# Optimization experiments

Hardware: AMD Instinct MI355X
Metric: run time of the kernel (lower is better)

The kernel has to match this reference:

```python
import jax, jax.numpy as jnp
import numpy as np

B, H, W, C = 8, 128, 128, 192
NH, WS, SHIFT = 6, 8, 4
N = WS * WS          # tokens per window = 64
NWIN = (H // WS) * (W // WS)  # 256 windows per image
SCALE = (C // NH) ** -0.5
EPS = 1e-5

# ---- relative position index (static, numpy) ----
_c = np.stack(np.meshgrid(np.arange(WS), np.arange(WS), indexing='ij')).reshape(2, -1)
_r = (_c[:, :, None] - _c[:, None, :]).transpose(1, 2, 0).astype(np.int64)
_r[..., 0] += WS - 1
_r[..., 1] += WS - 1
_r[..., 0] *= 2 * WS - 1
REL_IDX = jnp.asarray(_r.sum(-1))  # (N, N) in [0, (2*WS-1)**2)

# ---- shifted-window attention mask (static, numpy) ----
_img = np.zeros((H, W))
_cnt = 0
for hs in (slice(0, -WS), slice(-WS, -SHIFT), slice(-SHIFT, None)):
    for ws_ in (slice(0, -WS), slice(-WS, -SHIFT), slice(-SHIFT, None)):
        _img[hs, ws_] = _cnt
        _cnt += 1
_img = _img.reshape(H // WS, WS, W // WS, WS).transpose(0, 2, 1, 3).reshape(-1, N)
_m = _img[:, None, :] - _img[:, :, None]
ATTN_MASK = jnp.asarray(np.where(_m != 0, -100.0, 0.0).astype(np.float32))  # (NWIN, N, N)


def layer_norm(x, w, b):
    mu = x.mean(-1, keepdims=True)
    var = ((x - mu) ** 2).mean(-1, keepdims=True)  # biased variance
    return (x - mu) / jnp.sqrt(var + EPS) * w + b


def window_partition(x):
    # (B, H, W, C) -> (B*NWIN, N, C)
    x = x.reshape(B, H // WS, WS, W // WS, WS, C)
    return x.transpose(0, 1, 3, 2, 4, 5).reshape(B * NWIN, N, C)


def window_reverse(w_):
    # (B*NWIN, N, C) -> (B, H, W, C)
    x = w_.reshape(B, H // WS, W // WS, WS, WS, C)
    return x.transpose(0, 1, 3, 2, 4, 5).reshape(B, H, W, C)


def setup_inputs() -> dict:
    key = jax.random.key(0)
    ks = jax.random.split(key, 6)
    return {
        'x': jax.random.normal(ks[0], (B, H * W, C), jnp.float32),
        'ln1_w': jnp.ones((C,), jnp.float32),
        'ln1_b': jnp.zeros((C,), jnp.float32),
        'qkv_w': jax.random.normal(ks[1], (C, 3 * C), jnp.float32) * 0.02,
        'qkv_b': jnp.zeros((3 * C,), jnp.float32),
        'rpb_table': jax.random.normal(ks[2], ((2 * WS - 1) ** 2, NH), jnp.float32) * 0.02,
        'proj_w': jax.random.normal(ks[3], (C, C), jnp.float32) * 0.02,
        'proj_b': jnp.zeros((C,), jnp.float32),
        'ln2_w': jnp.ones((C,), jnp.float32),
        'ln2_b': jnp.zeros((C,), jnp.float32),
        'fc1_w': jax.random.normal(ks[4], (C, 4 * C), jnp.float32) * 0.02,
        'fc1_b': jnp.zeros((4 * C,), jnp.float32),
        'fc2_w': jax.random.normal(ks[5], (4 * C, C), jnp.float32) * 0.02,
        'fc2_b': jnp.zeros((C,), jnp.float32),
    }


def reference(x, ln1_w, ln1_b, qkv_w, qkv_b, rpb_table, proj_w, proj_b,
              ln2_w, ln2_b, fc1_w, fc1_b, fc2_w, fc2_b):
    shortcut = x
    h = layer_norm(x, ln1_w, ln1_b).reshape(B, H, W, C)
    # cyclic shift
    h = jnp.roll(h, shift=(-SHIFT, -SHIFT), axis=(1, 2))
    xw = window_partition(h)  # (B*NWIN, N, C)

    qkv = (xw @ qkv_w + qkv_b).reshape(B * NWIN, N, 3, NH, C // NH)
    q, k, v = [qkv[:, :, i].transpose(0, 2, 1, 3) for i in range(3)]  # (Bn, NH, N, hd)
    attn = jnp.einsum('bhqd,bhkd->bhqk', q * SCALE, k)  # (Bn, NH, N, N)

    rel_bias = rpb_table[REL_IDX].transpose(2, 0, 1)  # (NH, N, N)
    attn = attn + rel_bias[None]
    # shift mask: broadcast per window
    attn = attn.reshape(B, NWIN, NH, N, N) + ATTN_MASK[None, :, None]
    attn = jax.nn.softmax(attn.reshape(B * NWIN, NH, N, N), axis=-1)

    out = jnp.einsum('bhqk,bhkd->bhqd', attn, v)
    out = out.transpose(0, 2, 1, 3).reshape(B * NWIN, N, C)
    out = out @ proj_w + proj_b

    h = window_reverse(out)
    h = jnp.roll(h, shift=(SHIFT, SHIFT), axis=(1, 2)).reshape(B, H * W, C)
    x = shortcut + h

    # MLP
    m = layer_norm(x, ln2_w, ln2_b)
    m = jax.nn.gelu(m @ fc1_w + fc1_b, approximate=False) @ fc2_w + fc2_b
    return x + m
```

## Files before the change

kernel.cpp:

```cpp
#include <hip/hip_runtime.h>
#include <math.h>

typedef _Float16 f16;
typedef _Float16 f16x8 __attribute__((ext_vector_type(8)));
typedef float f32x4 __attribute__((ext_vector_type(4)));

namespace {
constexpr int Hh = 128, Ww = 128, Cc = 192;
constexpr int NHh = 6;
constexpr int Nn = 64, HDd = 32;
constexpr int SH = 4;
constexpr int Mrows = 131072;
constexpr int NWINtot = 2048;
constexpr float LNEPS = 1e-5f;
constexpr float QSCALE = 0.17677669529663687f;
}

__device__ __forceinline__ void ldsload16(const void* g, void* l) {
  __builtin_amdgcn_global_load_lds(
      (const __attribute__((address_space(1))) void*)g,
      (__attribute__((address_space(3))) void*)l, 16, 0, 0);
}

__device__ __forceinline__ int win_row_to_src(int m) {
  int tok = m & 63;
  int wi  = m >> 6;
  int ww = wi & 15, wh = (wi >> 4) & 15, b = wi >> 8;
  int r = (wh << 3) + (tok >> 3);
  int c = (ww << 3) + (tok & 7);
  int ro = (r + SH) & (Hh - 1);
  int co = (c + SH) & (Ww - 1);
  return (b << 14) + (ro << 7) + co;
}

template <int GATHER>
__global__ __launch_bounds__(256) void ln_prep_kernel(
    const float* __restrict__ X, const float* __restrict__ lnw,
    const float* __restrict__ lnb, f16* __restrict__ outh, int m0) {
  __shared__ float xr[16][192];
  __shared__ float smu[16], srs[16];
  __shared__ int src[16];
  const int t = threadIdx.x;
  const int r0 = blockIdx.x * 16;
  if (t < 16) {
    int m = m0 + r0 + t;
    src[t] = GATHER ? win_row_to_src(m) : m;
  }
  __syncthreads();
#pragma unroll
  for (int it = 0; it < 3; ++it) {
    int f = t + it * 256;
    int row = f / 48, c4 = f - row * 48;
    float4 v = *(const float4*)&X[(size_t)src[row] * 192 + c4 * 4];
    *(float4*)&xr[row][c4 * 4] = v;
  }
  __syncthreads();
  {
    const int lane = t & 63, w = t >> 6;
    const int g = lane >> 4, li = lane & 15;
    const int row = w * 4 + g;
    float s = 0.f, s2 = 0.f;
#pragma unroll
    for (int j = 0; j < 12; ++j) {
      float v = xr[row][li + j * 16];
      s += v; s2 += v * v;
    }
#pragma unroll
    for (int off = 1; off < 16; off <<= 1) {
      s += __shfl_xor(s, off);
      s2 += __shfl_xor(s2, off);
    }
    if (li == 0) {
      float m = s * (1.f / 192.f);
      smu[row] = m;
      srs[row] = rsqrtf(s2 * (1.f / 192.f) - m * m + LNEPS);
    }
  }
  __syncthreads();
#pragma unroll
  for (int it = 0; it < 2; ++it) {
    int c = t + it * 256;
    if (c < 384) {
      int e0 = c * 8;
      int row = e0 / 192, col = e0 - row * 192;
      float mu_ = smu[row], rs_ = srs[row];
      f16x8 o;
#pragma unroll
      for (int j = 0; j < 8; ++j) {
        float v = (xr[row][col + j] - mu_) * rs_ * lnw[col + j] + lnb[col + j];
        o[j] = (f16)v;
      }
      *(f16x8*)&outh[(size_t)(m0 + r0) * 192 + e0] = o;
    }
  }
}

__global__ __launch_bounds__(256) void rpb_expand_kernel(
    const float* __restrict__ rpb, float* __restrict__ biasF2) {
  int t = blockIdx.x * 256 + threadIdx.x;
  if (t >= NHh * 4 * 4 * 64 * 4) return;
  int r = t & 3, lane = (t >> 2) & 63, jt = (t >> 8) & 3, it = (t >> 10) & 3, h = t >> 12;
  int row = it * 16 + (lane >> 4) * 4 + r;
  int col = jt * 16 + (lane & 15);
  int dh = (row >> 3) - (col >> 3) + 7;
  int dw = (row & 7) - (col & 7) + 7;
  biasF2[t] = rpb[(dh * 15 + dw) * NHh + h];
}

__global__ __launch_bounds__(256) void wconv_frag(
    const float* __restrict__ W, f16* __restrict__ Wf, int K, int N) {
  int tid = blockIdx.x * 256 + threadIdx.x;
  if (tid >= K * N) return;
  int e = tid & 7, lane = (tid >> 3) & 63, f = tid >> 9;
  int NKT = K >> 5;
  int kt = f % NKT, nt = f / NKT;
  int k = kt * 32 + ((lane >> 4) << 3) + e;
  int n = nt * 16 + (lane & 15);
  Wf[tid] = (f16)W[(size_t)k * N + n];
}

template <int KDIM, int NDIM, int EMODE>
__global__ __launch_bounds__(512, 2) void gemm_mfma16(
    const f16* __restrict__ Abase, const f16* __restrict__ Bf,
    const float* __restrict__ bias, const float* __restrict__ resid,
    void* __restrict__ outp, int m0a, int m0e, int nbx) {
  constexpr int NCH = KDIM / 192;
  constexpr int NKT = KDIM / 32;
  __shared__ __align__(16) char lds[48 * 1024];

  const int tid = threadIdx.x;
  const int lane = tid & 63;
  const int wid = tid >> 6;
  const int wr = wid & 1, wc = wid >> 1;
  const int l15 = lane & 15, g2 = lane >> 4;

  int b = blockIdx.x;
  const int nb = gridDim.x;
  if ((nb & 7) == 0) b = (b & 7) * (nb >> 3) + (b >> 3);
  const int bx = b % nbx;
  const int by = b / nbx;
  const int bn = bx * 192;
  const int bm = by * 128;
  const int nt0 = bx * 12 + wc * 3;

  const int srow = tid >> 2;
  const int kq = tid & 3;
  const int sg = srow >> 4;
  const int slot = srow & 15;
  const f16* arow = Abase + (size_t)(m0a + bm + srow) * KDIM;

  f32x4 acc[4][3];
#pragma unroll
  for (int i = 0; i < 4; ++i)
#pragma unroll
    for (int j = 0; j < 3; ++j) acc[i][j] = (f32x4){0.f, 0.f, 0.f, 0.f};

  for (int c = 0; c < NCH; ++c) {
    if (c) __syncthreads();
#pragma unroll
    for (int u = 0; u < 6; ++u) {
      int ch = kq + u * 4;
      f16x8 v = *(const f16x8*)&arow[c * 192 + ch * 8];
      int ks = ch >> 2, h = ch & 3;
      *(f16x8*)(lds + (ks * 8 + sg) * 1024 + (slot + h * 16) * 16) = v;
    }
    __syncthreads();

#pragma unroll
    for (int ks = 0; ks < 6; ++ks) {
      f16x8 bf[3];
#pragma unroll
      for (int ni = 0; ni < 3; ++ni)
        bf[ni] = *(const f16x8*)&Bf[
            (((size_t)(nt0 + ni) * NKT + (c * 6 + ks)) << 9) + (lane << 3)];
#pragma unroll
      for (int mi = 0; mi < 4; ++mi) {
        f16x8 ah = *(const f16x8*)(lds + (ks * 8 + wr * 4 + mi) * 1024 + lane * 16);
#pragma unroll
        for (int ni = 0; ni < 3; ++ni)
          acc[mi][ni] = __builtin_amdgcn_mfma_f32_16x16x32_f16(ah, bf[ni], acc[mi][ni], 0, 0, 0);
      }
    }
  }

#pragma unroll
  for (int mi = 0; mi < 4; ++mi) {
#pragma unroll
    for (int ni = 0; ni < 3; ++ni) {
      int col = bn + wc * 48 + ni * 16 + l15;
      float bcol = bias[col];
#pragma unroll
      for (int r = 0; r < 4; ++r) {
        int ml = bm + wr * 64 + mi * 16 + g2 * 4 + r;
        float v = acc[mi][ni][r] + bcol;
        if (EMODE == 0) {
          ((f16*)outp)[(size_t)ml * NDIM + col] = (f16)v;
        } else {
          int dst = win_row_to_src(m0e + ml);
          ((float*)outp)[(size_t)dst * NDIM + col] = v + resid[(size_t)dst * NDIM + col];
        }
      }
    }
  }
}

__global__ __launch_bounds__(256, 2) void mlp_fused(
    const f16* __restrict__ oh, const f16* __restrict__ W1f,
    const f16* __restrict__ W2f, const float* __restrict__ b1,
    const float* __restrict__ b2, float* __restrict__ out) {
  __shared__ __align__(16) char ldsA[24 * 1024];
  __shared__ __align__(16) char ldsH[24 * 1024];

  const int tid = threadIdx.x;
  const int lane = tid & 63;
  const int wc = tid >> 6;
  const int l15 = lane & 15, g2 = lane >> 4;
  const int bm = blockIdx.x * 64;

  {
    const f16* src = oh + (size_t)(bm + wc * 16 + l15) * 192 + g2 * 8;
#pragma unroll
    for (int ks = 0; ks < 6; ++ks)
      ldsload16(src + ks * 32, &ldsA[(ks * 4 + wc) * 1024]);
  }

  f32x4 acc2[4][3];
#pragma unroll
  for (int i = 0; i < 4; ++i)
#pragma unroll
    for (int j = 0; j < 3; ++j) acc2[i][j] = (f32x4){0.f, 0.f, 0.f, 0.f};

  __syncthreads();

  for (int hc = 0; hc < 4; ++hc) {
    f32x4 acc1[4][3];
#pragma unroll
    for (int i = 0; i < 4; ++i)
#pragma unroll
      for (int j = 0; j < 3; ++j) acc1[i][j] = (f32x4){0.f, 0.f, 0.f, 0.f};
#pragma unroll
    for (int ks = 0; ks < 6; ++ks) {
      f16x8 bf[3];
#pragma unroll
      for (int ni = 0; ni < 3; ++ni)
        bf[ni] = *(const f16x8*)&W1f[
            (((size_t)(hc * 12 + wc * 3 + ni) * 6 + ks) << 9) + (lane << 3)];
#pragma unroll
      for (int mi = 0; mi < 4; ++mi) {
        f16x8 ah = *(const f16x8*)(ldsA + (ks * 4 + mi) * 1024 + lane * 16);
#pragma unroll
        for (int ni = 0; ni < 3; ++ni)
          acc1[mi][ni] = __builtin_amdgcn_mfma_f32_16x16x32_f16(ah, bf[ni], acc1[mi][ni], 0, 0, 0);
      }
    }
#pragma unroll
    for (int mi = 0; mi < 4; ++mi)
#pragma unroll
      for (int ni = 0; ni < 3; ++ni) {
        float bcol = b1[hc * 192 + wc * 48 + ni * 16 + l15];
#pragma unroll
        for (int r = 0; r < 4; ++r) {
          float v = acc1[mi][ni][r] + bcol;
          float u = v * (1.f + 0.044715f * v * v);
          float ex = __expf(-1.5957691216f * u);
          v = v * __builtin_amdgcn_rcpf(1.f + ex);
          int row = mi * 16 + g2 * 4 + r;
          int col = wc * 48 + ni * 16 + l15;
          *(f16*)(ldsH + ((col >> 5) * 4 + mi) * 1024 +
                  ((row & 15) + ((col >> 3) & 3) * 16) * 16 + (col & 7) * 2) = (f16)v;
        }
      }
    __syncthreads();

#pragma unroll
    for (int ks = 0; ks < 6; ++ks) {
      f16x8 bf[3];
#pragma unroll
      for (int ni = 0; ni < 3; ++ni)
        bf[ni] = *(const f16x8*)&W2f[
            (((size_t)(wc * 3 + ni) * 24 + hc * 6 + ks) << 9) + (lane << 3)];
#pragma unroll
      for (int mi = 0; mi < 4; ++mi) {
        f16x8 ah = *(const f16x8*)(ldsH + (ks * 4 + mi) * 1024 + lane * 16);
#pragma unroll
        for (int ni = 0; ni < 3; ++ni)
          acc2[mi][ni] = __builtin_amdgcn_mfma_f32_16x16x32_f16(ah, bf[ni], acc2[mi][ni], 0, 0, 0);
      }
    }
    __syncthreads();
  }

#pragma unroll
  for (int mi = 0; mi < 4; ++mi)
#pragma unroll
    for (int ni = 0; ni < 3; ++ni) {
      int col = wc * 48 + ni * 16 + l15;
      float bcol = b2[col];
#pragma unroll
      for (int r = 0; r < 4; ++r) {
        int ml = bm + mi * 16 + g2 * 4 + r;
        out[(size_t)ml * 192 + col] = acc2[mi][ni][r] + bcol + out[(size_t)ml * 192 + col];
      }
    }
}

__global__ __launch_bounds__(384) void attn_mfma(
    const f16* __restrict__ qkv, const float* __restrict__ biasF2,
    f16* __restrict__ out, int w0) {
  __shared__ f16 Vt[192 * 64];
  __shared__ f16 Pb[NHh][64 * 64];
  const int t = threadIdx.x;
  const int h = t >> 6;
  const int lane = t & 63;
  const int g = lane >> 4, l15 = lane & 15;
  const int wl = blockIdx.x;
  const f16* base = qkv + (size_t)wl * 64 * 576;

  {
    const f16* vr = base + (size_t)lane * 576 + 384 + h * 32;
    f16x8 vv[4];
#pragma unroll
    for (int u = 0; u < 4; ++u) vv[u] = *(const f16x8*)&vr[u * 8];
    const int c = lane >> 3, e7 = lane & 7;
#pragma unroll
    for (int u = 0; u < 4; ++u)
#pragma unroll
      for (int e = 0; e < 8; ++e) {
        int d = h * 32 + u * 8 + e;
        Vt[d * 64 + ((c ^ e) << 3) + e7] = vv[u][e];
      }
  }

  f16x8 qf[4], kf[4];
#pragma unroll
  for (int it = 0; it < 4; ++it)
    qf[it] = *(const f16x8*)&base[(size_t)(it * 16 + l15) * 576 + h * 32 + g * 8];
#pragma unroll
  for (int jt = 0; jt < 4; ++jt)
    kf[jt] = *(const f16x8*)&base[(size_t)(jt * 16 + l15) * 576 + 192 + h * 32 + g * 8];

  f32x4 S[4][4];
#pragma unroll
  for (int it = 0; it < 4; ++it)
#pragma unroll
    for (int jt = 0; jt < 4; ++jt) S[it][jt] = (f32x4){0.f, 0.f, 0.f, 0.f};
#pragma unroll
  for (int it = 0; it < 4; ++it)
#pragma unroll
    for (int jt = 0; jt < 4; ++jt)
      S[it][jt] = __builtin_amdgcn_mfma_f32_16x16x32_f16(qf[it], kf[jt], S[it][jt], 0, 0, 0);

  const int wi = (w0 + wl) & 255;
  const int wh = wi >> 4, wwc = wi & 15;
  int regj[4];
#pragma unroll
  for (int jt = 0; jt < 4; ++jt) {
    int col = jt * 16 + l15;
    int rj = wh * 8 + (col >> 3), cj = wwc * 8 + (col & 7);
    regj[jt] = (rj < 120 ? 0 : rj < 124 ? 1 : 2) * 3 + (cj < 120 ? 0 : cj < 124 ? 1 : 2);
  }
#pragma unroll
  for (int it = 0; it < 4; ++it) {
    int regi[4];
#pragma unroll
    for (int r = 0; r < 4; ++r) {
      int row = it * 16 + g * 4 + r;
      int ri = wh * 8 + (row >> 3), ci = wwc * 8 + (row & 7);
      regi[r] = (ri < 120 ? 0 : ri < 124 ? 1 : 2) * 3 + (ci < 120 ? 0 : ci < 124 ? 1 : 2);
    }
#pragma unroll
    for (int jt = 0; jt < 4; ++jt) {
      f32x4 bb = *(const f32x4*)&biasF2[(((h * 4 + it) * 4 + jt) * 64 + lane) * 4];
#pragma unroll
      for (int r = 0; r < 4; ++r) {
        float v = S[it][jt][r] * QSCALE + bb[r];
        if (regi[r] != regj[jt]) v -= 100.f;
        S[it][jt][r] = v;
      }
    }
  }

#pragma unroll
  for (int it = 0; it < 4; ++it) {
#pragma unroll
    for (int r = 0; r < 4; ++r) {
      float m = fmaxf(fmaxf(S[it][0][r], S[it][1][r]), fmaxf(S[it][2][r], S[it][3][r]));
#pragma unroll
      for (int off = 1; off < 16; off <<= 1) m = fmaxf(m, __shfl_xor(m, off));
#pragma unroll
      for (int jt = 0; jt < 4; ++jt) S[it][jt][r] = __expf(S[it][jt][r] - m);
    }
  }

  f16* pb = &Pb[h][0];
#pragma unroll
  for (int it = 0; it < 4; ++it)
#pragma unroll
    for (int jt = 0; jt < 4; ++jt)
#pragma unroll
      for (int r = 0; r < 4; ++r) {
        int row = it * 16 + g * 4 + r;
        int cs = (jt * 2 + (l15 >> 3)) ^ (row & 7);
        pb[row * 64 + cs * 8 + (l15 & 7)] = (f16)S[it][jt][r];
      }

  f32x4 O[4][2], Ssum[4];
#pragma unroll
  for (int it = 0; it < 4; ++it) {
    O[it][0] = (f32x4){0.f, 0.f, 0.f, 0.f};
    O[it][1] = (f32x4){0.f, 0.f, 0.f, 0.f};
    Ssum[it] = (f32x4){0.f, 0.f, 0.f, 0.f};
  }
  f16x8 ones;
#pragma unroll
  for (int e = 0; e < 8; ++e) ones[e] = (f16)1.f;
#pragma unroll
  for (int jh = 0; jh < 2; ++jh) {
    const int csw = ((jh * 4 + g) ^ (l15 & 7)) << 3;
    f16x8 pf[4], vf[2];
#pragma unroll
    for (int it = 0; it < 4; ++it) pf[it] = *(const f16x8*)&pb[(it * 16 + l15) * 64 + csw];
#pragma unroll
    for (int dt = 0; dt < 2; ++dt) vf[dt] = *(const f16x8*)&Vt[(h * 32 + dt * 16 + l15) * 64 + csw];
#pragma unroll
    for (int it = 0; it < 4; ++it) {
      O[it][0] = __builtin_amdgcn_mfma_f32_16x16x32_f16(pf[it], vf[0], O[it][0], 0, 0, 0);
      O[it][1] = __builtin_amdgcn_mfma_f32_16x16x32_f16(pf[it], vf[1], O[it][1], 0, 0, 0);
      Ssum[it] = __builtin_amdgcn_mfma_f32_16x16x32_f16(pf[it], ones, Ssum[it], 0, 0, 0);
    }
  }

#pragma unroll
  for (int it = 0; it < 4; ++it) {
    f32x4 rin;
#pragma unroll
    for (int r = 0; r < 4; ++r) rin[r] = 1.f / Ssum[it][r];
#pragma unroll
    for (int dt = 0; dt < 2; ++dt)
#pragma unroll
      for (int r = 0; r < 4; ++r) {
        int row = it * 16 + g * 4 + r;
        out[(size_t)(wl * 64 + row) * 192 + h * 32 + dt * 16 + l15] =
            (f16)(O[it][dt][r] * rin[r]);
      }
  }
}

extern "C" void kernel_launch(void* const* d_in, const int* in_sizes, int n_in,
                              void* d_out, int out_size, void* d_ws, size_t ws_size,
                              hipStream_t stream) {
  const float* x     = (const float*)d_in[0];
  const float* ln1w  = (const float*)d_in[1];
  const float* ln1b  = (const float*)d_in[2];
  const float* qkvw  = (const float*)d_in[3];
  const float* qkvb  = (const float*)d_in[4];
  const float* rpb   = (const float*)d_in[5];
  const float* projw = (const float*)d_in[6];
  const float* projb = (const float*)d_in[7];
  const float* ln2w  = (const float*)d_in[8];
  const float* ln2b  = (const float*)d_in[9];
  const float* fc1w  = (const float*)d_in[10];
  const float* fc1b  = (const float*)d_in[11];
  const float* fc2w  = (const float*)d_in[12];
  const float* fc2b  = (const float*)d_in[13];
  float* out = (float*)d_out;

  char* ws = (char*)d_ws;
  float* biasF2 = (float*)ws;
  f16* qkvwF = (f16*)(ws + 98304);
  f16* projwF = (f16*)(ws + 319488);
  f16* fc1wF = (f16*)(ws + 393216);
  f16* fc2wF = (f16*)(ws + 688128);
  f16* xh    = (f16*)(ws + 983040);
  f16* oh    = (f16*)(ws + 983040 + 50331648);
  char* big  = ws + 983040 + 2 * 50331648;
  size_t R = ws_size > (size_t)(983040 + 2 * 50331648)
                 ? ws_size - (983040 + 2 * 50331648) : 0;

  long long wch = (long long)(R / 98304);
  if (wch > NWINtot) wch = NWINtot;
  wch &= ~1LL;
  if (wch < 2) wch = 2;

  wconv_frag<<<432, 256, 0, stream>>>(qkvw, qkvwF, 192, 576);
  wconv_frag<<<144, 256, 0, stream>>>(projw, projwF, 192, 192);
  wconv_frag<<<576, 256, 0, stream>>>(fc1w, fc1wF, 192, 768);
  wconv_frag<<<576, 256, 0, stream>>>(fc2w, fc2wF, 768, 192);
  rpb_expand_kernel<<<96, 256, 0, stream>>>(rpb, biasF2);

  ln_prep_kernel<1><<<Mrows / 16, 256, 0, stream>>>(x, ln1w, ln1b, xh, 0);

  f16* qkvc = (f16*)big;
  f16* aoc  = (f16*)(big + (size_t)wch * 73728);
  for (int w = 0; w < NWINtot; w += (int)wch) {
    int cur = (NWINtot - w < (int)wch) ? (NWINtot - w) : (int)wch;
    int ny = cur * 64 / 128;
    gemm_mfma16<192, 576, 0><<<3 * ny, 512, 0, stream>>>(
        xh, qkvwF, qkvb, nullptr, qkvc, w * 64, 0, 3);
    attn_mfma<<<cur, 384, 0, stream>>>(qkvc, biasF2, aoc, w);
    gemm_mfma16<192, 192, 2><<<ny, 512, 0, stream>>>(
        aoc, projwF, projb, x, out, 0, w * 64, 1);
  }

  ln_prep_kernel<0><<<Mrows / 16, 256, 0, stream>>>(out, ln2w, ln2b, oh, 0);

  mlp_fused<<<Mrows / 64, 256, 0, stream>>>(oh, fc1wF, fc2wF, fc1b, fc2b, out);
}
```

Baseline: 431.6 us.

## Fuse output projection and residual add into the window attention kernel

The attention kernel now writes its normalized per-head outputs into shared memory in MFMA fragment layout. After that it runs the 64x192x192 output projection itself, with each wave producing 32 columns, and adds bias and residual while scattering rows back to unshifted positions. This drops the separate projection GEMM launch and the fp16 round trip of the attention output through global memory. It also frees workspace, so more windows fit per chunk. The cost is more work and registers inside the attention kernel, plus projection weight fragments read from global memory by every block.

```diff
diff --git a/kernel.cpp b/kernel.cpp
--- a/kernel.cpp
+++ b/kernel.cpp
@@ -192,13 +192,7 @@
 #pragma unroll
       for (int r = 0; r < 4; ++r) {
         int ml = bm + wr * 64 + mi * 16 + g2 * 4 + r;
-        float v = acc[mi][ni][r] + bcol;
-        if (EMODE == 0) {
-          ((f16*)outp)[(size_t)ml * NDIM + col] = (f16)v;
-        } else {
-          int dst = win_row_to_src(m0e + ml);
-          ((float*)outp)[(size_t)dst * NDIM + col] = v + resid[(size_t)dst * NDIM + col];
-        }
+        ((f16*)outp)[(size_t)ml * NDIM + col] = (f16)(acc[mi][ni][r] + bcol);
       }
     }
   }
@@ -306,7 +300,8 @@
 
 __global__ __launch_bounds__(384) void attn_mfma(
     const f16* __restrict__ qkv, const float* __restrict__ biasF2,
-    f16* __restrict__ out, int w0) {
+    const f16* __restrict__ Wpf, const float* __restrict__ pb_,
+    const float* __restrict__ resid, float* __restrict__ out, int w0) {
   __shared__ f16 Vt[192 * 64];
   __shared__ f16 Pb[NHh][64 * 64];
   const int t = threadIdx.x;
@@ -430,18 +425,63 @@
     }
   }
 
-#pragma unroll
-  for (int it = 0; it < 4; ++it) {
-    f32x4 rin;
-#pragma unroll
-    for (int r = 0; r < 4; ++r) rin[r] = 1.f / Ssum[it][r];
-#pragma unroll
-    for (int dt = 0; dt < 2; ++dt)
-#pragma unroll
-      for (int r = 0; r < 4; ++r) {
-        int row = it * 16 + g * 4 + r;
-        out[(size_t)(wl * 64 + row) * 192 + h * 32 + dt * 16 + l15] =
-            (f16)(O[it][dt][r] * rin[r]);
+  __syncthreads();
+
+  {
+    char* Ao = (char*)&Pb[0][0];
+#pragma unroll
+    for (int it = 0; it < 4; ++it) {
+      f32x4 rin;
+#pragma unroll
+      for (int r = 0; r < 4; ++r) rin[r] = 1.f / Ssum[it][r];
+#pragma unroll
+      for (int dt = 0; dt < 2; ++dt) {
+        int hh = dt * 2 + (l15 >> 3);
+        int e = l15 & 7;
+#pragma unroll
+        for (int r = 0; r < 4; ++r) {
+          *(f16*)(Ao + (h * 4 + it) * 1024 + ((g * 4 + r) + hh * 16) * 16 + e * 2) =
+              (f16)(O[it][dt][r] * rin[r]);
+        }
+      }
+    }
+  }
+  __syncthreads();
+
+  {
+    const char* Ao = (const char*)&Pb[0][0];
+    f32x4 acc[4][2];
+#pragma unroll
+    for (int i = 0; i < 4; ++i) {
+      acc[i][0] = (f32x4){0.f, 0.f, 0.f, 0.f};
+      acc[i][1] = (f32x4){0.f, 0.f, 0.f, 0.f};
+    }
+#pragma unroll
+    for (int ks = 0; ks < 6; ++ks) {
+      f16x8 bf[2];
+#pragma unroll
+      for (int ni = 0; ni < 2; ++ni)
+        bf[ni] = *(const f16x8*)&Wpf[(((size_t)(h * 2 + ni) * 6 + ks) << 9) + (lane << 3)];
+#pragma unroll
+      for (int it = 0; it < 4; ++it) {
+        f16x8 ah = *(const f16x8*)(Ao + (ks * 4 + it) * 1024 + lane * 16);
+#pragma unroll
+        for (int ni = 0; ni < 2; ++ni)
+          acc[it][ni] = __builtin_amdgcn_mfma_f32_16x16x32_f16(ah, bf[ni], acc[it][ni], 0, 0, 0);
+      }
+    }
+#pragma unroll
+    for (int it = 0; it < 4; ++it)
+#pragma unroll
+      for (int ni = 0; ni < 2; ++ni) {
+        int col = h * 32 + ni * 16 + l15;
+        float bcol = pb_[col];
+#pragma unroll
+        for (int r = 0; r < 4; ++r) {
+          int ml = it * 16 + g * 4 + r;
+          int dst = win_row_to_src((w0 + wl) * 64 + ml);
+          out[(size_t)dst * 192 + col] = acc[it][ni][r] + bcol + resid[(size_t)dst * 192 + col];
+        }
       }
   }
 }
@@ -477,7 +517,7 @@
   size_t R = ws_size > (size_t)(983040 + 2 * 50331648)
                  ? ws_size - (983040 + 2 * 50331648) : 0;
 
-  long long wch = (long long)(R / 98304);
+  long long wch = (long long)(R / 73728);
   if (wch > NWINtot) wch = NWINtot;
   wch &= ~1LL;
   if (wch < 2) wch = 2;
@@ -491,15 +531,12 @@
   ln_prep_kernel<1><<<Mrows / 16, 256, 0, stream>>>(x, ln1w, ln1b, xh, 0);
 
   f16* qkvc = (f16*)big;
-  f16* aoc  = (f16*)(big + (size_t)wch * 73728);
   for (int w = 0; w < NWINtot; w += (int)wch) {
     int cur = (NWINtot - w < (int)wch) ? (NWINtot - w) : (int)wch;
     int ny = cur * 64 / 128;
     gemm_mfma16<192, 576, 0><<<3 * ny, 512, 0, stream>>>(
         xh, qkvwF, qkvb, nullptr, qkvc, w * 64, 0, 3);
-    attn_mfma<<<cur, 384, 0, stream>>>(qkvc, biasF2, aoc, w);
-    gemm_mfma16<192, 192, 2><<<ny, 512, 0, stream>>>(
-        aoc, projwF, projb, x, out, 0, w * 64, 1);
+    attn_mfma<<<cur, 384, 0, stream>>>(qkvc, biasF2, projwF, projb, x, out, w);
   }
 
   ln_prep_kernel<0><<<Mrows / 16, 256, 0, stream>>>(out, ln2w, ln2b, oh, 0);
```

Result: faster. 381.9 us (-11.5%).
